# Kernel tuning notes

Measured on AMD Instinct MI355X. Metric: run time of the kernel, lower is better.

Reference implementation:

```python
import jax, jax.numpy as jnp
import numpy as np

N_POINTS = 64
N_DIM = 2 * N_POINTS          # 128
N_CONTROL = 2
FC = [1024, 1024]
DT = 0.1
ELEMS_A = 4 * N_POINTS        # 256 (computed but unused, matching original)
ELEMS_B = N_DIM * N_CONTROL   # 256


def setup_inputs() -> dict:
    key = jax.random.key(0)
    ks = jax.random.split(key, 8)
    B, T = 4096, 64
    states = jax.random.normal(ks[0], (B, T, N_DIM), dtype=jnp.float32)
    actions = jax.random.normal(ks[1], (B, T, N_CONTROL), dtype=jnp.float32)
    d_in = N_DIM + N_CONTROL  # 130
    scale = lambda fan_in: 1.0 / np.sqrt(fan_in)
    W1 = jax.random.normal(ks[2], (d_in, FC[0]), dtype=jnp.float32) * scale(d_in)
    b1 = jnp.zeros((FC[0],), dtype=jnp.float32)
    W2 = jax.random.normal(ks[3], (FC[0], FC[1]), dtype=jnp.float32) * scale(FC[0])
    b2 = jnp.zeros((FC[1],), dtype=jnp.float32)
    W3 = jax.random.normal(ks[4], (FC[1], ELEMS_A + ELEMS_B), dtype=jnp.float32) * scale(FC[1])
    b3 = jnp.zeros((ELEMS_A + ELEMS_B,), dtype=jnp.float32)
    return {"states": states, "actions": actions,
            "W1": W1, "b1": b1, "W2": W2, "b2": b2, "W3": W3, "b3": b3}


def reference(states, actions, W1, b1, W2, b2, W3, b3):
    # states: [B, T, n_dim], actions: [B, T, 2]
    s0 = states[:, 0]  # [B, n_dim]
    actions_t = jnp.swapaxes(actions, 0, 1)  # [T, B, 2]

    def step(s, a):
        z = jnp.concatenate([s, a], axis=1)          # [B, n_dim+2]
        z = jax.nn.relu(z @ W1 + b1)
        z = jax.nn.relu(z @ W2 + b2)
        params = z @ W3 + b3                          # [B, elems_A + elems_B]
        # A_t params (params[:, :ELEMS_A]) are computed but unused in the original update.
        B_params = params[:, ELEMS_A:]                # [B, 4*n_points]
        Bmat = B_params.reshape(-1, N_DIM, N_CONTROL) # block rows: [B, 2*n_points, 2]
        s_next = s + jnp.einsum('bnc,bc->bn', Bmat, a) * DT
        return s_next, s_next

    _, traj = jax.lax.scan(step, s0, actions_t)       # traj: [T, B, n_dim]
    gen = jnp.concatenate([s0[:, None], jnp.swapaxes(traj, 0, 1)], axis=1)
    return gen  # [B, T+1, n_dim]
```

## Files before the change

kernel.cpp:

```cpp
#include <hip/hip_runtime.h>
#include <stdint.h>

#define B_SZ 4096
#define T_SZ 64
#define ND   128
#define HID  1024
#define PO   256

typedef __attribute__((ext_vector_type(8))) short bf16x8;
typedef __attribute__((ext_vector_type(4))) float f32x4;

__device__ __forceinline__ unsigned short f2bf(float x) {
  unsigned int u = __float_as_uint(x);
  u += 0x7fffu + ((u >> 16) & 1u);
  return (unsigned short)(u >> 16);
}
__device__ __forceinline__ float bf2f(unsigned short h) {
  return __uint_as_float(((unsigned int)h) << 16);
}

__device__ __forceinline__ void g2lds(const void* g, void* l) {
  __builtin_amdgcn_global_load_lds(
      (const __attribute__((address_space(1))) unsigned int*)g,
      (__attribute__((address_space(3))) unsigned int*)l, 16, 0, 0);
}

template <int BM, int BN, int MT, int NT, int EPI>
__global__ __launch_bounds__(256, 2) void gemm_split(
    const unsigned short* __restrict__ Ahi, const unsigned short* __restrict__ Alo,
    const unsigned short* __restrict__ Bhi, const unsigned short* __restrict__ Blo,
    const float* __restrict__ bias, int K, int ldc,
    const float* __restrict__ a_t, const float* __restrict__ w1r,
    unsigned short* __restrict__ Zhi, unsigned short* __restrict__ Zlo,
    float* __restrict__ S, float* __restrict__ gen, int t) {
  constexpr int BK = 32;
  constexpr int ABYTES = BM * BK * 2;
  constexpr int BBYTES = BN * BK * 2;
  constexpr int RA = (ABYTES + 4095) / 4096;
  constexpr int RB = (BBYTES + 4095) / 4096;
  constexpr int WN_WAVES = BN / (NT * 16);
  constexpr int WM_WAVES = BM / (MT * 16);
  static_assert(WM_WAVES * WN_WAVES == 4, "4 waves per block");
  __shared__ __attribute__((aligned(16))) unsigned short AsH[2][BM * BK];
  __shared__ __attribute__((aligned(16))) unsigned short AsL[2][BM * BK];
  __shared__ __attribute__((aligned(16))) unsigned short BsH[2][BN * BK];
  __shared__ __attribute__((aligned(16))) unsigned short BsL[2][BN * BK];

  const int tid  = threadIdx.x;
  const int lane = tid & 63;
  const int wave = tid >> 6;
  const int wm = (wave / WN_WAVES) * (MT * 16);
  const int wn = (wave % WN_WAVES) * (NT * 16);
  const int m0 = blockIdx.x * BM;
  const int n0 = blockIdx.y * BN;
  const size_t Kb = (size_t)K * 2;

  size_t gA[RA], gB[RB];
  int lA[RA], lB[RB];
#pragma unroll
  for (int r = 0; r < RA; ++r) {
    int L = (r * 256 + tid) * 16;
    lA[r] = L;
    int row = L >> 6;
    int sc  = ((L >> 4) & 3) ^ ((row >> 1) & 3);
    gA[r] = (size_t)(m0 + row) * Kb + (sc << 4);
  }
#pragma unroll
  for (int r = 0; r < RB; ++r) {
    int L = (r * 256 + tid) * 16;
    lB[r] = L;
    int row = L >> 6;
    int sc  = ((L >> 4) & 3) ^ ((row >> 1) & 3);
    gB[r] = (size_t)(n0 + row) * Kb + (sc << 4);
  }

  f32x4 acc[MT][NT] = {};
  const char* Ah = (const char*)Ahi;
  const char* Al = (const char*)Alo;
  const char* Bh = (const char*)Bhi;
  const char* Bl = (const char*)Blo;
  char* asH = (char*)AsH; char* asL = (char*)AsL;
  char* bsH = (char*)BsH; char* bsL = (char*)BsL;

  const int kIt = K / BK;

#pragma unroll
  for (int r = 0; r < RA; ++r)
    if (ABYTES % 4096 == 0 || lA[r] < ABYTES) {
      g2lds(Ah + gA[r], asH + lA[r]);
      g2lds(Al + gA[r], asL + lA[r]);
    }
#pragma unroll
  for (int r = 0; r < RB; ++r)
    if (BBYTES % 4096 == 0 || lB[r] < BBYTES) {
      g2lds(Bh + gB[r], bsH + lB[r]);
      g2lds(Bl + gB[r], bsL + lB[r]);
    }

  int cur = 0;
  for (int it = 0; it < kIt; ++it) {
    __syncthreads();

    if (it + 1 < kIt) {
      const size_t kadd = (size_t)(it + 1) * (BK * 2);
      const int la = (cur ^ 1) * ABYTES;
      const int lb = (cur ^ 1) * BBYTES;
#pragma unroll
      for (int r = 0; r < RA; ++r)
        if (ABYTES % 4096 == 0 || lA[r] < ABYTES) {
          g2lds(Ah + gA[r] + kadd, asH + la + lA[r]);
          g2lds(Al + gA[r] + kadd, asL + la + lA[r]);
        }
#pragma unroll
      for (int r = 0; r < RB; ++r)
        if (BBYTES % 4096 == 0 || lB[r] < BBYTES) {
          g2lds(Bh + gB[r] + kadd, bsH + lb + lB[r]);
          g2lds(Bl + gB[r] + kadd, bsL + lb + lB[r]);
        }
    }

    bf16x8 fa_h[MT], fa_l[MT], fb_h[NT], fb_l[NT];
#pragma unroll
    for (int mt = 0; mt < MT; ++mt) {
      int r = wm + mt * 16 + (lane & 15);
      int c = (lane >> 4) ^ ((r >> 1) & 3);
      int off = r * BK + c * 8;
      fa_h[mt] = *(const bf16x8*)&AsH[cur][off];
      fa_l[mt] = *(const bf16x8*)&AsL[cur][off];
    }
#pragma unroll
    for (int nt = 0; nt < NT; ++nt) {
      int r = wn + nt * 16 + (lane & 15);
      int c = (lane >> 4) ^ ((r >> 1) & 3);
      int off = r * BK + c * 8;
      fb_h[nt] = *(const bf16x8*)&BsH[cur][off];
      fb_l[nt] = *(const bf16x8*)&BsL[cur][off];
    }
#pragma unroll
    for (int mt = 0; mt < MT; ++mt)
#pragma unroll
      for (int nt = 0; nt < NT; ++nt) {
        acc[mt][nt] = __builtin_amdgcn_mfma_f32_16x16x32_bf16(fa_h[mt], fb_h[nt], acc[mt][nt], 0, 0, 0);
        acc[mt][nt] = __builtin_amdgcn_mfma_f32_16x16x32_bf16(fa_l[mt], fb_h[nt], acc[mt][nt], 0, 0, 0);
        acc[mt][nt] = __builtin_amdgcn_mfma_f32_16x16x32_bf16(fa_h[mt], fb_l[nt], acc[mt][nt], 0, 0, 0);
      }
    cur ^= 1;
  }

#pragma unroll
  for (int mt = 0; mt < MT; ++mt) {
    const int mb = m0 + wm + mt * 16 + ((lane >> 4) << 2);
    float a0v[4], a1v[4];
    if (EPI == 1 || EPI == 3) {
#pragma unroll
      for (int r = 0; r < 4; ++r) {
        a0v[r] = a_t[(mb + r) * 2];
        a1v[r] = a_t[(mb + r) * 2 + 1];
      }
    }
#pragma unroll
    for (int nt = 0; nt < NT; ++nt) {
      const int n = n0 + wn + nt * 16 + (lane & 15);
      const float bv = bias[n];
      float w0 = 0.f, w1 = 0.f;
      if (EPI == 1) { w0 = w1r[n]; w1 = w1r[HID + n]; }
#pragma unroll
      for (int r = 0; r < 4; ++r) {
        float v = acc[mt][nt][r] + bv;
        if (EPI == 3) {
          float vx = __shfl_xor(v, 1);
          if (!(lane & 1)) {
            const int b = mb + r;
            const int j = n >> 1;
            const float sv = S[b * ND + j] + (v * a0v[r] + vx * a1v[r]) * 0.1f;
            S[b * ND + j] = sv;
            unsigned short h = f2bf(sv);
            Zhi[b * ND + j] = h;
            Zlo[b * ND + j] = f2bf(sv - bf2f(h));
            gen[(size_t)b * ((T_SZ + 1) * ND) + (size_t)(t + 1) * ND + j] = sv;
          }
        } else {
          if (EPI == 1) v += a0v[r] * w0 + a1v[r] * w1;
          v = fmaxf(v, 0.f);
          unsigned short h = f2bf(v);
          const size_t idx = (size_t)(mb + r) * ldc + n;
          Zhi[idx] = h;
          Zlo[idx] = f2bf(v - bf2f(h));
        }
      }
    }
  }
}

__global__ void prep_kernel(
    const float* __restrict__ states, const float* __restrict__ actions,
    const float* __restrict__ W1, const float* __restrict__ W2,
    const float* __restrict__ W3,
    unsigned short* __restrict__ W1tH, unsigned short* __restrict__ W1tL,
    unsigned short* __restrict__ W2tH, unsigned short* __restrict__ W2tL,
    unsigned short* __restrict__ W3tH, unsigned short* __restrict__ W3tL,
    float* __restrict__ aT, float* __restrict__ s,
    unsigned short* __restrict__ sH, unsigned short* __restrict__ sL,
    float* __restrict__ gen) {
  const int tid = blockIdx.x * blockDim.x + threadIdx.x;
  const int stride = gridDim.x * blockDim.x;
  for (int i = tid; i < ND * HID; i += stride) {
    int k = i >> 10, j = i & 1023;
    float v = W1[i];
    unsigned short h = f2bf(v);
    W1tH[j * ND + k] = h;
    W1tL[j * ND + k] = f2bf(v - bf2f(h));
  }
  for (int i = tid; i < HID * HID; i += stride) {
    int k = i >> 10, j = i & 1023;
    float v = W2[i];
    unsigned short h = f2bf(v);
    W2tH[j * HID + k] = h;
    W2tL[j * HID + k] = f2bf(v - bf2f(h));
  }
  for (int i = tid; i < HID * PO; i += stride) {
    int k = i >> 8, j = i & 255;
    float v = W3[k * 512 + 256 + j];
    unsigned short h = f2bf(v);
    W3tH[j * HID + k] = h;
    W3tL[j * HID + k] = f2bf(v - bf2f(h));
  }
  for (int i = tid; i < B_SZ * T_SZ; i += stride) {
    int b = i >> 6, t = i & 63;
    float2 v = ((const float2*)actions)[i];
    ((float2*)aT)[t * B_SZ + b] = v;
  }
  for (int i = tid; i < B_SZ * ND; i += stride) {
    int b = i >> 7, n = i & 127;
    float v = states[(size_t)b * (T_SZ * ND) + n];
    s[i] = v;
    unsigned short h = f2bf(v);
    sH[i] = h;
    sL[i] = f2bf(v - bf2f(h));
    gen[(size_t)b * ((T_SZ + 1) * ND) + n] = v;
  }
}

extern "C" void kernel_launch(void* const* d_in, const int* in_sizes, int n_in,
                              void* d_out, int out_size, void* d_ws, size_t ws_size,
                              hipStream_t stream) {
  const float* states  = (const float*)d_in[0];
  const float* actions = (const float*)d_in[1];
  const float* W1 = (const float*)d_in[2];
  const float* b1 = (const float*)d_in[3];
  const float* W2 = (const float*)d_in[4];
  const float* b2 = (const float*)d_in[5];
  const float* W3 = (const float*)d_in[6];
  const float* b3 = (const float*)d_in[7];
  float* gen = (float*)d_out;

  char* w = (char*)d_ws;
  float*          s    = (float*)(w + 0);
  unsigned short* sH   = (unsigned short*)(w + (2ull << 20));
  unsigned short* sL   = (unsigned short*)(w + (3ull << 20));
  unsigned short* z1H  = (unsigned short*)(w + (4ull << 20));
  unsigned short* z1L  = (unsigned short*)(w + (12ull << 20));
  unsigned short* z2H  = (unsigned short*)(w + (20ull << 20));
  unsigned short* z2L  = (unsigned short*)(w + (28ull << 20));
  float*          aT   = (float*)(w + (40ull << 20));
  unsigned short* W1tH = (unsigned short*)(w + (42ull << 20));
  unsigned short* W1tL = (unsigned short*)(w + (42ull << 20) + 262144);
  unsigned short* W2tH = (unsigned short*)(w + (43ull << 20));
  unsigned short* W2tL = (unsigned short*)(w + (45ull << 20));
  unsigned short* W3tH = (unsigned short*)(w + (47ull << 20));
  unsigned short* W3tL = (unsigned short*)(w + (47ull << 20) + 524288);

  prep_kernel<<<2048, 256, 0, stream>>>(states, actions, W1, W2, W3,
      W1tH, W1tL, W2tH, W2tL, W3tH, W3tL, aT, s, sH, sL, gen);

  const float* w1r = W1 + 128 * 1024;
  for (int t = 0; t < 64; ++t) {
    const float* at = aT + (size_t)t * B_SZ * 2;
    gemm_split<128, 64, 4, 2, 1><<<dim3(32, 16), 256, 0, stream>>>(
        sH, sL, W1tH, W1tL, b1, 128, HID, at, w1r, z1H, z1L,
        (float*)nullptr, (float*)nullptr, 0);
    gemm_split<128, 64, 4, 2, 2><<<dim3(32, 16), 256, 0, stream>>>(
        z1H, z1L, W2tH, W2tL, b2, HID, HID, (const float*)nullptr,
        (const float*)nullptr, z2H, z2L, (float*)nullptr, (float*)nullptr, 0);
    gemm_split<64, 32, 2, 1, 3><<<dim3(64, 8), 256, 0, stream>>>(
        z2H, z2L, W3tH, W3tL, b3 + 256, HID, PO, at, (const float*)nullptr,
        sH, sL, s, gen, t);
  }
}
```

Baseline: 4.423 ms.

## Triple-buffer LDS tiles with two-deep async prefetch and partial vmcnt waits

Switches the split-bf16 GEMM mainloop from double to triple buffering. Two K-tiles are prefetched ahead, and each iteration waits only for the older group of global-to-LDS loads, using a per-thread vmcnt count instead of a full drain, followed by a raw s_barrier. This is meant to hide more global memory latency behind the MFMA work. In exchange it uses 1.5x the LDS, which may lower occupancy, and the correctness of the manual waitcnt depends on the per-thread load count matching the vmcnt immediates.

```diff
diff --git a/kernel.cpp b/kernel.cpp
--- a/kernel.cpp
+++ b/kernel.cpp
@@ -41,10 +41,10 @@
   constexpr int WN_WAVES = BN / (NT * 16);
   constexpr int WM_WAVES = BM / (MT * 16);
   static_assert(WM_WAVES * WN_WAVES == 4, "4 waves per block");
-  __shared__ __attribute__((aligned(16))) unsigned short AsH[2][BM * BK];
-  __shared__ __attribute__((aligned(16))) unsigned short AsL[2][BM * BK];
-  __shared__ __attribute__((aligned(16))) unsigned short BsH[2][BN * BK];
-  __shared__ __attribute__((aligned(16))) unsigned short BsL[2][BN * BK];
+  __shared__ __attribute__((aligned(16))) unsigned short AsH[3][BM * BK];
+  __shared__ __attribute__((aligned(16))) unsigned short AsL[3][BM * BK];
+  __shared__ __attribute__((aligned(16))) unsigned short BsH[3][BN * BK];
+  __shared__ __attribute__((aligned(16))) unsigned short BsL[3][BN * BK];
 
   const int tid  = threadIdx.x;
   const int lane = tid & 63;
@@ -74,6 +74,14 @@
     gB[r] = (size_t)(n0 + row) * Kb + (sc << 4);
   }
 
+  int myLoads = 0;
+#pragma unroll
+  for (int r = 0; r < RA; ++r)
+    if (ABYTES % 4096 == 0 || lA[r] < ABYTES) myLoads += 2;
+#pragma unroll
+  for (int r = 0; r < RB; ++r)
+    if (BBYTES % 4096 == 0 || lB[r] < BBYTES) myLoads += 2;
+
   f32x4 acc[MT][NT] = {};
   const char* Ah = (const char*)Ahi;
   const char* Al = (const char*)Alo;
@@ -84,41 +92,44 @@
 
   const int kIt = K / BK;
 
-#pragma unroll
-  for (int r = 0; r < RA; ++r)
-    if (ABYTES % 4096 == 0 || lA[r] < ABYTES) {
-      g2lds(Ah + gA[r], asH + lA[r]);
-      g2lds(Al + gA[r], asL + lA[r]);
-    }
-#pragma unroll
-  for (int r = 0; r < RB; ++r)
-    if (BBYTES % 4096 == 0 || lB[r] < BBYTES) {
-      g2lds(Bh + gB[r], bsH + lB[r]);
-      g2lds(Bl + gB[r], bsL + lB[r]);
-    }
-
-  int cur = 0;
+  auto stage = [&](int itS, int bsel) {
+    const size_t kadd = (size_t)itS * (BK * 2);
+    const int la = bsel * ABYTES;
+    const int lb = bsel * BBYTES;
+#pragma unroll
+    for (int r = 0; r < RA; ++r)
+      if (ABYTES % 4096 == 0 || lA[r] < ABYTES) {
+        g2lds(Ah + gA[r] + kadd, asH + la + lA[r]);
+        g2lds(Al + gA[r] + kadd, asL + la + lA[r]);
+      }
+#pragma unroll
+    for (int r = 0; r < RB; ++r)
+      if (BBYTES % 4096 == 0 || lB[r] < BBYTES) {
+        g2lds(Bh + gB[r] + kadd, bsH + lb + lB[r]);
+        g2lds(Bl + gB[r] + kadd, bsL + lb + lB[r]);
+      }
+  };
+
+  stage(0, 0);
+  if (kIt > 1) stage(1, 1);
+
   for (int it = 0; it < kIt; ++it) {
-    __syncthreads();
-
     if (it + 1 < kIt) {
-      const size_t kadd = (size_t)(it + 1) * (BK * 2);
-      const int la = (cur ^ 1) * ABYTES;
-      const int lb = (cur ^ 1) * BBYTES;
-#pragma unroll
-      for (int r = 0; r < RA; ++r)
-        if (ABYTES % 4096 == 0 || lA[r] < ABYTES) {
-          g2lds(Ah + gA[r] + kadd, asH + la + lA[r]);
-          g2lds(Al + gA[r] + kadd, asL + la + lA[r]);
-        }
-#pragma unroll
-      for (int r = 0; r < RB; ++r)
-        if (BBYTES % 4096 == 0 || lB[r] < BBYTES) {
-          g2lds(Bh + gB[r] + kadd, bsH + lb + lB[r]);
-          g2lds(Bl + gB[r] + kadd, bsL + lb + lB[r]);
-        }
-    }
-
+      switch (myLoads) {
+        case 6: asm volatile("s_waitcnt vmcnt(6)" ::: "memory"); break;
+        case 4: asm volatile("s_waitcnt vmcnt(4)" ::: "memory"); break;
+        case 2: asm volatile("s_waitcnt vmcnt(2)" ::: "memory"); break;
+        default: asm volatile("s_waitcnt vmcnt(0)" ::: "memory"); break;
+      }
+    } else {
+      asm volatile("s_waitcnt vmcnt(0)" ::: "memory");
+    }
+    __builtin_amdgcn_s_barrier();
+    __builtin_amdgcn_sched_barrier(0);
+
+    if (it + 2 < kIt) stage(it + 2, (it + 2) % 3);
+
+    const int cur = it % 3;
     bf16x8 fa_h[MT], fa_l[MT], fb_h[NT], fb_l[NT];
 #pragma unroll
     for (int mt = 0; mt < MT; ++mt) {
@@ -144,7 +155,6 @@
         acc[mt][nt] = __builtin_amdgcn_mfma_f32_16x16x32_bf16(fa_l[mt], fb_h[nt], acc[mt][nt], 0, 0, 0);
         acc[mt][nt] = __builtin_amdgcn_mfma_f32_16x16x32_bf16(fa_h[mt], fb_l[nt], acc[mt][nt], 0, 0, 0);
       }
-    cur ^= 1;
   }
 
 #pragma unroll
```

Measured after the change: 4.503 ms. About the same (+1.8%).
